# Kernel optimization log

Measured on AMD Instinct MI355X. Metric: run time of the kernel, lower is better.

Reference implementation:

```python
import jax, jax.numpy as jnp
import numpy as np

EMBED_DIM = 768
NUM_HEADS = 12
HEAD_SIZE = EMBED_DIM // NUM_HEADS


def setup_inputs() -> dict:
    key = jax.random.key(0)
    ks = jax.random.split(key, 9)
    B, S, D = 4, 2048, EMBED_DIM
    scale = 1.0 / np.sqrt(D)
    x = jax.random.normal(ks[0], (B, S, D), dtype=jnp.float32)
    # Linear params (torch nn.Linear: y = x @ W.T + b); store W as [in, out] for einsum
    Wq = jax.random.normal(ks[1], (D, D), dtype=jnp.float32) * scale
    bq = jnp.zeros((D,), dtype=jnp.float32)
    Wk = jax.random.normal(ks[2], (D, D), dtype=jnp.float32) * scale
    bk = jnp.zeros((D,), dtype=jnp.float32)
    Wv = jax.random.normal(ks[3], (D, D), dtype=jnp.float32) * scale
    bv = jnp.zeros((D,), dtype=jnp.float32)
    Wo = jax.random.normal(ks[4], (D, D), dtype=jnp.float32) * scale
    bo = jnp.zeros((D,), dtype=jnp.float32)
    return {"x": x, "Wq": Wq, "bq": bq, "Wk": Wk, "bk": bk,
            "Wv": Wv, "bv": bv, "Wo": Wo, "bo": bo}


def reference(x, Wq, bq, Wk, bk, Wv, bv, Wo, bo):
    B, S, D = x.shape
    H, hs = NUM_HEADS, HEAD_SIZE
    scale = hs ** (-0.5)
    # Projections
    Q = (x @ Wq + bq).reshape(B, S, H, hs)
    K = (x @ Wk + bk).reshape(B, S, H, hs)
    V = (x @ Wv + bv).reshape(B, S, H, hs)
    # Batched attention over all heads (equivalent to the per-head loop:
    # torch view splits last dim into H contiguous chunks; concat of per-head
    # outputs along -1 restores the same layout)
    scores = jnp.einsum('bqhd,bkhd->bhqk', Q, K) * scale  # [B,H,S,S]
    attn = jax.nn.softmax(scores, axis=-1)
    out = jnp.einsum('bhqk,bkhd->bqhd', attn, V).reshape(B, S, D)
    # Output projection; dropout is identity in eval mode
    return out @ Wo + bo
```

## Files before the change

kernel.cpp:

```cpp
#include <hip/hip_runtime.h>

typedef unsigned short ushort_t;
typedef __bf16 bf16x8 __attribute__((ext_vector_type(8)));
typedef float floatx4 __attribute__((ext_vector_type(4)));

__device__ inline ushort_t f2bf(float f) {
    __bf16 h = (__bf16)f;
    return __builtin_bit_cast(ushort_t, h);
}

__device__ inline void gload16(const void* g, void* l) {
    __builtin_amdgcn_global_load_lds((const __attribute__((address_space(1))) void*)g,
                                     (__attribute__((address_space(3))) void*)l, 16, 0, 0);
}

__global__ __launch_bounds__(256) void prep_kernel(
    const float* __restrict__ x, ushort_t* __restrict__ xbf,
    const float* __restrict__ W0, const float* __restrict__ W1,
    const float* __restrict__ W2, const float* __restrict__ W3,
    ushort_t* __restrict__ T0, ushort_t* __restrict__ T1,
    ushort_t* __restrict__ T2, ushort_t* __restrict__ T3) {
    int bx = blockIdx.x;
    int tid = threadIdx.x;
    if (bx < 2304) {
        __shared__ float t[32][33];
        int w = bx / 576, rem = bx % 576;
        const float* W; ushort_t* T;
        switch (w) {
            case 0: W = W0; T = T0; break;
            case 1: W = W1; T = T1; break;
            case 2: W = W2; T = T2; break;
            default: W = W3; T = T3; break;
        }
        int n0 = (rem / 24) * 32, k0 = (rem % 24) * 32;
        int tx = tid & 31, ty = tid >> 5;
        for (int i = 0; i < 4; ++i)
            t[ty + i * 8][tx] = W[(k0 + ty + i * 8) * 768 + n0 + tx];
        __syncthreads();
        for (int i = 0; i < 4; ++i)
            T[(n0 + ty + i * 8) * 768 + k0 + tx] = f2bf(t[tx][ty + i * 8]);
    } else {
        int i = ((bx - 2304) * 256 + tid) * 4;
        float4 v = *(const float4*)(x + i);
        ushort4 u;
        u.x = f2bf(v.x); u.y = f2bf(v.y); u.z = f2bf(v.z); u.w = f2bf(v.w);
        *(ushort4*)(xbf + i) = u;
    }
}

__global__ __launch_bounds__(256) void gemm_qkv(
    const ushort_t* __restrict__ A,
    const ushort_t* __restrict__ Tq, const ushort_t* __restrict__ Tk, const ushort_t* __restrict__ Tv,
    const float* __restrict__ bq, const float* __restrict__ bk, const float* __restrict__ bv,
    ushort_t* __restrict__ Qb, ushort_t* __restrict__ Kb, ushort_t* __restrict__ Vtb) {
    __shared__ ushort_t sh[128 * 64 + 64 * 64];
    ushort_t* As = sh;
    ushort_t* Bs = sh + 128 * 64;
    int tid = threadIdx.x;
    int m0 = blockIdx.x * 128;
    int by = blockIdx.y;
    int which = by / 12;
    int n0 = (by % 12) * 64;
    const ushort_t* Bt = which == 0 ? Tq : (which == 1 ? Tk : Tv);
    const float* bias = which == 0 ? bq : (which == 1 ? bk : bv);

    int wave = tid >> 6;
    int lane = tid & 63;
    int ln = tid & 15;
    int quad = (tid >> 4) & 3;
    int wm = wave * 32;
    int lr = lane >> 3;
    int lc = (lane & 7) * 8;

    floatx4 acc[2][4];
    floatx4 z = {0.f, 0.f, 0.f, 0.f};
    for (int i = 0; i < 2; ++i)
        for (int j = 0; j < 4; ++j) acc[i][j] = z;

    for (int kt = 0; kt < 12; ++kt) {
        int k0 = kt * 64;
        __syncthreads();
        for (int i = 0; i < 4; ++i) {
            int c = wave * 4 + i;
            gload16(&A[(m0 + c * 8 + lr) * 768 + k0 + lc], &As[c * 512]);
        }
        for (int i = 0; i < 2; ++i) {
            int c = wave * 2 + i;
            gload16(&Bt[(n0 + c * 8 + lr) * 768 + k0 + lc], &Bs[c * 512]);
        }
        __syncthreads();
        for (int ks = 0; ks < 2; ++ks) {
            bf16x8 a[2], b[4];
            for (int i = 0; i < 2; ++i)
                a[i] = *(const bf16x8*)&As[(wm + i * 16 + ln) * 64 + ks * 32 + quad * 8];
            for (int j = 0; j < 4; ++j)
                b[j] = *(const bf16x8*)&Bs[(j * 16 + ln) * 64 + ks * 32 + quad * 8];
            for (int i = 0; i < 2; ++i)
                for (int j = 0; j < 4; ++j)
                    acc[i][j] = __builtin_amdgcn_mfma_f32_16x16x32_bf16(a[i], b[j], acc[i][j], 0, 0, 0);
        }
    }

    const float QSCALE = 0.125f * 1.44269504088896f;
    if (which != 2) {
        for (int i = 0; i < 2; ++i) {
            for (int j = 0; j < 4; ++j) {
                int gn = n0 + j * 16 + ln;
                float bia = bias[gn];
                int h = gn >> 6, dd = gn & 63;
                for (int r = 0; r < 4; ++r) {
                    int gm = m0 + wm + i * 16 + quad * 4 + r;
                    int bb = gm >> 11, ss = gm & 2047;
                    float v = acc[i][j][r] + bia;
                    if (which == 0) {
                        Qb[((bb * 12 + h) * 2048 + ss) * 64 + dd] = f2bf(v * QSCALE);
                    } else {
                        Kb[((bb * 12 + h) * 2048 + ss) * 64 + dd] = f2bf(v);
                    }
                }
            }
        }
    } else {
        __syncthreads();
        ushort_t* tr = sh;
        for (int j = 0; j < 4; ++j) {
            int nl = j * 16 + ln;
            float bia = bias[n0 + nl];
            for (int i = 0; i < 2; ++i) {
                ushort4 u;
                u.x = f2bf(acc[i][j][0] + bia);
                u.y = f2bf(acc[i][j][1] + bia);
                u.z = f2bf(acc[i][j][2] + bia);
                u.w = f2bf(acc[i][j][3] + bia);
                *(ushort4*)&tr[nl * 136 + wm + i * 16 + quad * 4] = u;
            }
        }
        __syncthreads();
        int bb = m0 >> 11, ss0 = m0 & 2047;
        int head = by % 12;
        for (int p = 0; p < 4; ++p) {
            int n = p * 16 + (tid >> 4);
            int mc = (tid & 15) * 8;
            uint4 v = *(const uint4*)&tr[n * 136 + mc];
            *(uint4*)&Vtb[(size_t)((bb * 12 + head) * 64 + n) * 2048 + ss0 + mc] = v;
        }
    }
}

__global__ __launch_bounds__(256) void attn_kernel(
    const ushort_t* __restrict__ Qb, const ushort_t* __restrict__ Kb,
    const ushort_t* __restrict__ Vtb, ushort_t* __restrict__ Ob) {
    __shared__ ushort_t Ks[2][64 * 72];
    __shared__ ushort_t Vs[2][64 * 72];
    int tid = threadIdx.x;
    int qt = blockIdx.x;
    int bh = blockIdx.y;
    int wave = tid >> 6;
    int ln = tid & 15;
    int quad = (tid >> 4) & 3;
    int q0 = qt * 128 + wave * 32;

    const ushort_t* Qp = Qb + (size_t)bh * 2048 * 64;
    const ushort_t* Kp = Kb + (size_t)bh * 2048 * 64;
    const ushort_t* Vp = Vtb + (size_t)bh * 64 * 2048;

    bf16x8 bqf[2][2];
    for (int g = 0; g < 2; ++g)
        for (int ks = 0; ks < 2; ++ks)
            bqf[g][ks] = *(const bf16x8*)&Qp[(q0 + g * 16 + ln) * 64 + ks * 32 + quad * 8];

    int srow = tid >> 3;
    int c8 = tid & 7;
    int scol = c8 * 8;
    int u = c8 & 3;
    int vcol = (c8 >> 2) * 32 + (u & 1) * 16 + (u >> 1) * 4;

    uint4 kreg[2], vreg[2];

    for (int p = 0; p < 2; ++p) {
        kreg[p] = *(const uint4*)&Kp[(p * 32 + srow) * 64 + scol];
        vreg[p] = *(const uint4*)&Vp[(p * 32 + srow) * 2048 + scol];
    }
    for (int p = 0; p < 2; ++p) {
        *(uint4*)&Ks[0][(p * 32 + srow) * 72 + scol] = kreg[p];
        ushort_t* vb = &Vs[0][(p * 32 + srow) * 72 + vcol];
        *(uint2*)vb = make_uint2(vreg[p].x, vreg[p].y);
        *(uint2*)(vb + 8) = make_uint2(vreg[p].z, vreg[p].w);
    }
    __syncthreads();

    floatx4 o_acc[2][4];
    float lsum[2] = {0.f, 0.f};
    floatx4 z = {0.f, 0.f, 0.f, 0.f};
    for (int g = 0; g < 2; ++g)
        for (int m4 = 0; m4 < 4; ++m4) o_acc[g][m4] = z;

    for (int kt = 0; kt < 32; ++kt) {
        int cur = kt & 1;
        if (kt < 31) {
            for (int p = 0; p < 2; ++p) {
                kreg[p] = *(const uint4*)&Kp[((kt + 1) * 64 + p * 32 + srow) * 64 + scol];
                vreg[p] = *(const uint4*)&Vp[(p * 32 + srow) * 2048 + (kt + 1) * 64 + scol];
            }
        }

        const ushort_t* KsH = Ks[cur];
        const ushort_t* VsH = Vs[cur];

        bf16x8 ak[4][2];
        for (int m4 = 0; m4 < 4; ++m4)
            for (int ks = 0; ks < 2; ++ks)
                ak[m4][ks] = *(const bf16x8*)&KsH[(m4 * 16 + ln) * 72 + ks * 32 + quad * 8];

        floatx4 st[2][4];
        for (int g = 0; g < 2; ++g)
            for (int m4 = 0; m4 < 4; ++m4) {
                floatx4 s = z;
                s = __builtin_amdgcn_mfma_f32_16x16x32_bf16(ak[m4][0], bqf[g][0], s, 0, 0, 0);
                s = __builtin_amdgcn_mfma_f32_16x16x32_bf16(ak[m4][1], bqf[g][1], s, 0, 0, 0);
                st[g][m4] = s;
            }

        float pv[2][4][4];
        for (int g = 0; g < 2; ++g)
            for (int m4 = 0; m4 < 4; ++m4)
                for (int r = 0; r < 4; ++r) {
                    float e = __builtin_amdgcn_exp2f(st[g][m4][r]);
                    pv[g][m4][r] = e;
                    lsum[g] += e;
                }

        bf16x8 av[4][2];
        for (int m4 = 0; m4 < 4; ++m4)
            for (int c = 0; c < 2; ++c)
                av[m4][c] = *(const bf16x8*)&VsH[(m4 * 16 + ln) * 72 + c * 32 + quad * 8];

        for (int g = 0; g < 2; ++g) {
            bf16x8 bp[2];
            for (int c = 0; c < 2; ++c) {
                bf16x8 b;
                b[0] = (__bf16)pv[g][2 * c][0];
                b[1] = (__bf16)pv[g][2 * c][1];
                b[2] = (__bf16)pv[g][2 * c][2];
                b[3] = (__bf16)pv[g][2 * c][3];
                b[4] = (__bf16)pv[g][2 * c + 1][0];
                b[5] = (__bf16)pv[g][2 * c + 1][1];
                b[6] = (__bf16)pv[g][2 * c + 1][2];
                b[7] = (__bf16)pv[g][2 * c + 1][3];
                bp[c] = b;
            }
            for (int m4 = 0; m4 < 4; ++m4)
                for (int c = 0; c < 2; ++c)
                    o_acc[g][m4] = __builtin_amdgcn_mfma_f32_16x16x32_bf16(av[m4][c], bp[c], o_acc[g][m4], 0, 0, 0);
        }

        if (kt < 31) {
            int nxt = cur ^ 1;
            for (int p = 0; p < 2; ++p) {
                *(uint4*)&Ks[nxt][(p * 32 + srow) * 72 + scol] = kreg[p];
                ushort_t* vb = &Vs[nxt][(p * 32 + srow) * 72 + vcol];
                *(uint2*)vb = make_uint2(vreg[p].x, vreg[p].y);
                *(uint2*)(vb + 8) = make_uint2(vreg[p].z, vreg[p].w);
            }
        }
        __syncthreads();
    }

    for (int g = 0; g < 2; ++g) {
        lsum[g] += __shfl_xor(lsum[g], 16);
        lsum[g] += __shfl_xor(lsum[g], 32);
    }

    int b = bh / 12, h = bh % 12;
    for (int g = 0; g < 2; ++g) {
        float inv = 1.f / lsum[g];
        int token = b * 2048 + q0 + g * 16 + ln;
        for (int m4 = 0; m4 < 4; ++m4)
            for (int r = 0; r < 4; ++r)
                Ob[token * 768 + h * 64 + m4 * 16 + quad * 4 + r] = f2bf(o_acc[g][m4][r] * inv);
    }
}

__global__ __launch_bounds__(256) void gemm_out(
    const ushort_t* __restrict__ A, const ushort_t* __restrict__ Bt,
    const float* __restrict__ bias, float* __restrict__ out) {
    __shared__ ushort_t As[128 * 64];
    __shared__ ushort_t Bs[64 * 64];
    int tid = threadIdx.x;
    int m0 = blockIdx.x * 128;
    int n0 = blockIdx.y * 64;

    int wave = tid >> 6;
    int lane = tid & 63;
    int ln = tid & 15;
    int quad = (tid >> 4) & 3;
    int wm = wave * 32;
    int lr = lane >> 3;
    int lc = (lane & 7) * 8;

    floatx4 acc[2][4];
    floatx4 z = {0.f, 0.f, 0.f, 0.f};
    for (int i = 0; i < 2; ++i)
        for (int j = 0; j < 4; ++j) acc[i][j] = z;

    for (int kt = 0; kt < 12; ++kt) {
        int k0 = kt * 64;
        __syncthreads();
        for (int i = 0; i < 4; ++i) {
            int c = wave * 4 + i;
            gload16(&A[(m0 + c * 8 + lr) * 768 + k0 + lc], &As[c * 512]);
        }
        for (int i = 0; i < 2; ++i) {
            int c = wave * 2 + i;
            gload16(&Bt[(n0 + c * 8 + lr) * 768 + k0 + lc], &Bs[c * 512]);
        }
        __syncthreads();
        for (int ks = 0; ks < 2; ++ks) {
            bf16x8 a[2], b[4];
            for (int i = 0; i < 2; ++i)
                a[i] = *(const bf16x8*)&As[(wm + i * 16 + ln) * 64 + ks * 32 + quad * 8];
            for (int j = 0; j < 4; ++j)
                b[j] = *(const bf16x8*)&Bs[(j * 16 + ln) * 64 + ks * 32 + quad * 8];
            for (int i = 0; i < 2; ++i)
                for (int j = 0; j < 4; ++j)
                    acc[i][j] = __builtin_amdgcn_mfma_f32_16x16x32_bf16(a[i], b[j], acc[i][j], 0, 0, 0);
        }
    }

    for (int i = 0; i < 2; ++i) {
        for (int j = 0; j < 4; ++j) {
            int gn = n0 + j * 16 + ln;
            float bia = bias[gn];
            for (int r = 0; r < 4; ++r) {
                int gm = m0 + wm + i * 16 + quad * 4 + r;
                out[gm * 768 + gn] = acc[i][j][r] + bia;
            }
        }
    }
}

extern "C" void kernel_launch(void* const* d_in, const int* in_sizes, int n_in,
                              void* d_out, int out_size, void* d_ws, size_t ws_size,
                              hipStream_t stream) {
    const float* x  = (const float*)d_in[0];
    const float* Wq = (const float*)d_in[1];
    const float* bq = (const float*)d_in[2];
    const float* Wk = (const float*)d_in[3];
    const float* bk = (const float*)d_in[4];
    const float* Wv = (const float*)d_in[5];
    const float* bv = (const float*)d_in[6];
    const float* Wo = (const float*)d_in[7];
    const float* bo = (const float*)d_in[8];

    const int NTOK = 4 * 2048;
    const int NELT = NTOK * 768;
    const int WELT = 768 * 768;

    ushort_t* xbf = (ushort_t*)d_ws;
    ushort_t* Tq  = xbf + NELT;
    ushort_t* Tk  = Tq + WELT;
    ushort_t* Tv  = Tk + WELT;
    ushort_t* To  = Tv + WELT;
    ushort_t* Qb  = To + WELT;
    ushort_t* Kb  = Qb + NELT;
    ushort_t* Vtb = Kb + NELT;
    ushort_t* Ob  = Vtb + NELT;

    prep_kernel<<<8448, 256, 0, stream>>>(x, xbf, Wq, Wk, Wv, Wo, Tq, Tk, Tv, To);
    gemm_qkv<<<dim3(64, 36), 256, 0, stream>>>(xbf, Tq, Tk, Tv, bq, bk, bv, Qb, Kb, Vtb);
    attn_kernel<<<dim3(16, 48), 256, 0, stream>>>(Qb, Kb, Vtb, Ob);
    gemm_out<<<dim3(64, 12), 256, 0, stream>>>(Ob, To, bo, (float*)d_out);
}
```

Measured before the change: 224.7 us.

## Enlarge QKV GEMM tile to 128x128 and stage Q/K epilogue through LDS

After: 240.5 us. 7.0% more time.

```diff
diff --git a/kernel.cpp b/kernel.cpp
--- a/kernel.cpp
+++ b/kernel.cpp
@@ -53,14 +53,14 @@
     const ushort_t* __restrict__ Tq, const ushort_t* __restrict__ Tk, const ushort_t* __restrict__ Tv,
     const float* __restrict__ bq, const float* __restrict__ bk, const float* __restrict__ bv,
     ushort_t* __restrict__ Qb, ushort_t* __restrict__ Kb, ushort_t* __restrict__ Vtb) {
-    __shared__ ushort_t sh[128 * 64 + 64 * 64];
+    __shared__ ushort_t sh[2 * 128 * 64];
     ushort_t* As = sh;
     ushort_t* Bs = sh + 128 * 64;
     int tid = threadIdx.x;
     int m0 = blockIdx.x * 128;
     int by = blockIdx.y;
-    int which = by / 12;
-    int n0 = (by % 12) * 64;
+    int which = by / 6;
+    int n0 = (by % 6) * 128;
     const ushort_t* Bt = which == 0 ? Tq : (which == 1 ? Tk : Tv);
     const float* bias = which == 0 ? bq : (which == 1 ? bk : bv);
 
@@ -68,13 +68,14 @@
     int lane = tid & 63;
     int ln = tid & 15;
     int quad = (tid >> 4) & 3;
-    int wm = wave * 32;
+    int wr = (wave >> 1) * 64;
+    int wc = (wave & 1) * 64;
     int lr = lane >> 3;
     int lc = (lane & 7) * 8;
 
-    floatx4 acc[2][4];
+    floatx4 acc[4][4];
     floatx4 z = {0.f, 0.f, 0.f, 0.f};
-    for (int i = 0; i < 2; ++i)
+    for (int i = 0; i < 4; ++i)
         for (int j = 0; j < 4; ++j) acc[i][j] = z;
 
     for (int kt = 0; kt < 12; ++kt) {
@@ -83,66 +84,75 @@
         for (int i = 0; i < 4; ++i) {
             int c = wave * 4 + i;
             gload16(&A[(m0 + c * 8 + lr) * 768 + k0 + lc], &As[c * 512]);
-        }
-        for (int i = 0; i < 2; ++i) {
-            int c = wave * 2 + i;
             gload16(&Bt[(n0 + c * 8 + lr) * 768 + k0 + lc], &Bs[c * 512]);
         }
         __syncthreads();
         for (int ks = 0; ks < 2; ++ks) {
-            bf16x8 a[2], b[4];
-            for (int i = 0; i < 2; ++i)
-                a[i] = *(const bf16x8*)&As[(wm + i * 16 + ln) * 64 + ks * 32 + quad * 8];
+            bf16x8 a[4], b[4];
+            for (int i = 0; i < 4; ++i)
+                a[i] = *(const bf16x8*)&As[(wr + i * 16 + ln) * 64 + ks * 32 + quad * 8];
             for (int j = 0; j < 4; ++j)
-                b[j] = *(const bf16x8*)&Bs[(j * 16 + ln) * 64 + ks * 32 + quad * 8];
-            for (int i = 0; i < 2; ++i)
+                b[j] = *(const bf16x8*)&Bs[(wc + j * 16 + ln) * 64 + ks * 32 + quad * 8];
+            for (int i = 0; i < 4; ++i)
                 for (int j = 0; j < 4; ++j)
                     acc[i][j] = __builtin_amdgcn_mfma_f32_16x16x32_bf16(a[i], b[j], acc[i][j], 0, 0, 0);
         }
     }
 
     const float QSCALE = 0.125f * 1.44269504088896f;
+    __syncthreads();
     if (which != 2) {
-        for (int i = 0; i < 2; ++i) {
-            for (int j = 0; j < 4; ++j) {
-                int gn = n0 + j * 16 + ln;
-                float bia = bias[gn];
-                int h = gn >> 6, dd = gn & 63;
-                for (int r = 0; r < 4; ++r) {
-                    int gm = m0 + wm + i * 16 + quad * 4 + r;
-                    int bb = gm >> 11, ss = gm & 2047;
-                    float v = acc[i][j][r] + bia;
-                    if (which == 0) {
-                        Qb[((bb * 12 + h) * 2048 + ss) * 64 + dd] = f2bf(v * QSCALE);
-                    } else {
-                        Kb[((bb * 12 + h) * 2048 + ss) * 64 + dd] = f2bf(v);
+        ushort_t* QK = which == 0 ? Qb : Kb;
+        float scale = which == 0 ? QSCALE : 1.0f;
+        ushort_t* tr = sh;
+        for (int p = 0; p < 2; ++p) {
+            if ((wave >> 1) == p) {
+                for (int i = 0; i < 4; ++i)
+                    for (int j = 0; j < 4; ++j) {
+                        int ddp = wc + j * 16 + ln;
+                        float bia = bias[n0 + ddp];
+                        int rbase = (i * 16 + quad * 4) * 140 + ddp;
+                        for (int r = 0; r < 4; ++r)
+                            tr[rbase + r * 140] = f2bf((acc[i][j][r] + bia) * scale);
                     }
-                }
-            }
+            }
+            __syncthreads();
+            int row = tid >> 2, seg = tid & 3;
+            int gm = m0 + p * 64 + row;
+            int bb = gm >> 11, ss = gm & 2047;
+            int h = (n0 >> 6) + (seg >> 1);
+            int ddl = (seg & 1) * 32;
+            ushort_t* dst = &QK[((size_t)(bb * 12 + h) * 2048 + ss) * 64 + ddl];
+            const ushort_t* src = &tr[row * 140 + seg * 32];
+            for (int k = 0; k < 4; ++k)
+                *(uint4*)&dst[k * 8] = *(const uint4*)&src[k * 8];
+            __syncthreads();
         }
     } else {
-        __syncthreads();
         ushort_t* tr = sh;
-        for (int j = 0; j < 4; ++j) {
-            int nl = j * 16 + ln;
-            float bia = bias[n0 + nl];
-            for (int i = 0; i < 2; ++i) {
-                ushort4 u;
-                u.x = f2bf(acc[i][j][0] + bia);
-                u.y = f2bf(acc[i][j][1] + bia);
-                u.z = f2bf(acc[i][j][2] + bia);
-                u.w = f2bf(acc[i][j][3] + bia);
-                *(ushort4*)&tr[nl * 136 + wm + i * 16 + quad * 4] = u;
-            }
-        }
-        __syncthreads();
         int bb = m0 >> 11, ss0 = m0 & 2047;
-        int head = by % 12;
-        for (int p = 0; p < 4; ++p) {
-            int n = p * 16 + (tid >> 4);
-            int mc = (tid & 15) * 8;
-            uint4 v = *(const uint4*)&tr[n * 136 + mc];
-            *(uint4*)&Vtb[(size_t)((bb * 12 + head) * 64 + n) * 2048 + ss0 + mc] = v;
+        for (int p = 0; p < 2; ++p) {
+            if ((wave & 1) == p) {
+                for (int i = 0; i < 4; ++i)
+                    for (int j = 0; j < 4; ++j) {
+                        int nl = j * 16 + ln;
+                        float bia = bias[n0 + p * 64 + nl];
+                        ushort4 u;
+                        u.x = f2bf(acc[i][j][0] + bia);
+                        u.y = f2bf(acc[i][j][1] + bia);
+                        u.z = f2bf(acc[i][j][2] + bia);
+                        u.w = f2bf(acc[i][j][3] + bia);
+                        *(ushort4*)&tr[nl * 140 + wr + i * 16 + quad * 4] = u;
+                    }
+            }
+            __syncthreads();
+            int n = tid >> 2, seg = tid & 3;
+            int h = (n0 >> 6) + p;
+            const ushort_t* src = &tr[n * 140 + seg * 32];
+            ushort_t* dst = &Vtb[(size_t)((bb * 12 + h) * 64 + n) * 2048 + ss0 + seg * 32];
+            for (int k = 0; k < 4; ++k)
+                *(uint4*)&dst[k * 8] = *(const uint4*)&src[k * 8];
+            __syncthreads();
         }
     }
 }
@@ -367,7 +377,7 @@
     ushort_t* Ob  = Vtb + NELT;
 
     prep_kernel<<<8448, 256, 0, stream>>>(x, xbf, Wq, Wk, Wv, Wo, Tq, Tk, Tv, To);
-    gemm_qkv<<<dim3(64, 36), 256, 0, stream>>>(xbf, Tq, Tk, Tv, bq, bk, bv, Qb, Kb, Vtb);
+    gemm_qkv<<<dim3(64, 18), 256, 0, stream>>>(xbf, Tq, Tk, Tv, bq, bk, bv, Qb, Kb, Vtb);
     attn_kernel<<<dim3(16, 48), 256, 0, stream>>>(Qb, Kb, Vtb, Ob);
     gemm_out<<<dim3(64, 12), 256, 0, stream>>>(Ob, To, bo, (float*)d_out);
 }
```
